# Kernel tuning notes

Hardware: AMD Instinct MI355X
Metric: run time of the kernel (lower is better)

Reference implementation:

```python
import jax, jax.numpy as jnp
import numpy as np

N = 50000          # particles
E = 800000         # edges (avg degree 16)
IN_CH = 64
OUT_CH = 64
KH = 4             # kernel height
KW_HALF = 2        # stored half-width; full width = 4 after antisymmetrization
R = 0.1            # window support radius


def setup_inputs() -> dict:
    key = jax.random.key(0)
    k0, k1, k2, k3, k4 = jax.random.split(key, 5)
    features = jax.random.normal(k0, (N, IN_CH), dtype=jnp.float32)
    receivers = jax.random.randint(k1, (E,), 0, N)
    a = jax.random.randint(k2, (E,), 0, N)  # sender indices
    relative_positions = jax.random.uniform(k3, (E, 2), jnp.float32, -R, R)
    window_support = jnp.float32(R)
    # hk.initializers.RandomUniform(-0.05, 0.05)
    kernel = jax.random.uniform(k4, (KH, KW_HALF, IN_CH, OUT_CH), jnp.float32, -0.05, 0.05)
    bias = jnp.zeros((OUT_CH,), jnp.float32)
    return {"features": features, "receivers": receivers,
            "relative_positions": relative_positions,
            "window_support": window_support, "a": a,
            "kernel": kernel, "bias": bias}


def _continuous_conv(kernel_full, receivers, relative_positions, window_support,
                     features, senders):
    # kernel_full: [kh, kw, in, out]; bilinear interpolation (4 aggregation points)
    kh, kw, in_ch, out_ch = kernel_full.shape
    T = kh * kw
    n = features.shape[0]
    # normalized relative position in [-1, 1]
    u = jnp.clip(relative_positions / window_support, -1.0, 1.0)  # [E,2]
    gx = (u[:, 0] + 1.0) * 0.5 * (kh - 1)
    gy = (u[:, 1] + 1.0) * 0.5 * (kw - 1)
    x0 = jnp.clip(jnp.floor(gx), 0, kh - 2)
    y0 = jnp.clip(jnp.floor(gy), 0, kw - 2)
    fx = gx - x0
    fy = gy - y0
    x0i = x0.astype(jnp.int32)
    y0i = y0.astype(jnp.int32)
    # bilinear corner weights and flat kernel-tap indices  [E,4]
    w = jnp.stack([(1 - fx) * (1 - fy), (1 - fx) * fy,
                   fx * (1 - fy), fx * fy], axis=1)
    taps = jnp.stack([x0i * kw + y0i, x0i * kw + y0i + 1,
                      (x0i + 1) * kw + y0i, (x0i + 1) * kw + y0i + 1], axis=1)
    # smooth window function on normalized radius
    r2 = jnp.sum(u * u, axis=1)
    win = jnp.maximum(1.0 - r2, 0.0) ** 3  # [E]
    # gather sender features, apply window
    g = features[senders] * win[:, None]              # [E,in]
    wf = w[:, :, None] * g[:, None, :]                # [E,4,in]
    # scatter-aggregate into per-(receiver, kernel-tap) buckets
    seg = (receivers[:, None] * T + taps).reshape(-1)  # [E*4]
    A = jax.ops.segment_sum(wf.reshape(-1, in_ch), seg, num_segments=n * T)
    A = A.reshape(n, T, in_ch)
    # contract with kernel taps: out[n,o] = sum_t,i A[n,t,i] K[t,i,o]
    return jnp.einsum('nti,tio->no', A, kernel_full.reshape(T, in_ch, out_ch))


def reference(features, receivers, relative_positions, window_support, a,
              kernel, bias):
    # antisymmetrize kernel: [kh, 2*kw_half, in, out]
    kernel_full = jnp.concatenate([kernel, -jnp.flip(kernel, axis=(0, 1))], axis=1)
    out = _continuous_conv(kernel_full, receivers, relative_positions,
                           window_support, features, a)
    return out + bias
```

## Files before the change

kernel.cpp:

```cpp
#include <hip/hip_runtime.h>
#include <hip/hip_bf16.h>


#define T_TAPS 16
#define BUCKET 64

typedef unsigned short u16;
typedef short s16x8 __attribute__((ext_vector_type(8)));
typedef u16 u16x8 __attribute__((ext_vector_type(8)));
typedef float f32x2 __attribute__((ext_vector_type(2)));
typedef float f32x4 __attribute__((ext_vector_type(4)));

static __device__ __forceinline__ u16 f2bf(float x) {
    union { float f; unsigned u; } v; v.f = x;
    unsigned r = v.u + 0x7FFF + ((v.u >> 16) & 1);
    return (u16)(r >> 16);
}

__global__ __launch_bounds__(256) void ascc_setup(
    u16* __restrict__ KfT, const float* __restrict__ kern,
    int* __restrict__ cnt, int Nn)
{
    int b = blockIdx.x;
    if (b < 256) {
        int idx = b * 256 + threadIdx.x;
        int o = idx >> 10;
        int k = idx & 1023;
        int i = k >> 4, t = k & 15;
        int x = t >> 2, y = t & 3;
        float val;
        if (y < 2) val =  kern[(((x * 2 + y) * 64) + i) * 64 + o];
        else       val = -kern[((((3 - x) * 2 + (3 - y)) * 64) + i) * 64 + o];
        KfT[(size_t)o * 1024 + k] = f2bf(val);
    } else {
        int i = (b - 256) * 256 + threadIdx.x;
        if (i < Nn) cnt[i] = 0;
    }
}

__global__ __launch_bounds__(256) void ascc_fillprep(
    float4* __restrict__ rec,
    int* __restrict__ cnt, const int* __restrict__ receivers,
    const float* __restrict__ relpos, const float* __restrict__ wsup,
    const int* __restrict__ senders, int E)
{
    int e = blockIdx.x * 256 + threadIdx.x;
    if (e >= E) return;
    int r = receivers[e];
    int p = atomicAdd(&cnt[r], 1);
    if (p >= BUCKET) return;

    float ws = wsup[0];
    float2 rp = *(const float2*)(relpos + 2 * e);
    float u0 = fminf(fmaxf(rp.x / ws, -1.f), 1.f);
    float u1 = fminf(fmaxf(rp.y / ws, -1.f), 1.f);
    float gx = (u0 + 1.f) * 1.5f;
    float gy = (u1 + 1.f) * 1.5f;
    float x0f = fminf(fmaxf(floorf(gx), 0.f), 2.f);
    float y0f = fminf(fmaxf(floorf(gy), 0.f), 2.f);
    float fx = gx - x0f, fy = gy - y0f;
    int x0i = (int)x0f, y0i = (int)y0f;
    float r2 = u0 * u0 + u1 * u1;
    float win = fmaxf(1.f - r2, 0.f);
    win = win * win * win;
    float wx[4], wy[4];
    #pragma unroll
    for (int k = 0; k < 4; ++k)
        wx[k] = win * ((k == x0i) ? (1.f - fx) : ((k == x0i + 1) ? fx : 0.f));
    #pragma unroll
    for (int k = 0; k < 4; ++k)
        wy[k] = (k == y0i) ? (1.f - fy) : ((k == y0i + 1) ? fy : 0.f);

    union { int i; float f; } sv; sv.i = senders[e];
    size_t slot = (size_t)r * BUCKET + p;
    rec[2 * slot]     = make_float4(wx[0], wx[1], wx[2], wx[3]);
    rec[2 * slot + 1] = make_float4(wy[0], wy[1], wy[2], sv.f);
}

__global__ __launch_bounds__(256) void ascc_accum(
    u16* __restrict__ Abf,
    const float* __restrict__ features,
    const int* __restrict__ cnt,
    const float4* __restrict__ rec,
    int Nn)
{
    int lane = threadIdx.x & 63;
    int r = blockIdx.x * 4 + (threadIdx.x >> 6);
    if (r >= Nn) return;

    f32x2 acc[8];
    #pragma unroll
    for (int t = 0; t < 8; ++t) acc[t] = (f32x2){0.f, 0.f};

    int n = cnt[r];
    n = (n < BUCKET) ? n : BUCKET;
    const float4* rbase = rec + (size_t)r * (2 * BUCKET);

    #pragma unroll 1
    for (int j = 0; j < n; j += 4) {
        float4 ra[4], rb[4];
        float g[4];
        #pragma unroll
        for (int q = 0; q < 4; ++q) {
            int jj = j + q;
            int jc = (jj < n) ? jj : (n - 1);
            ra[q] = rbase[2 * jc];
            rb[q] = rbase[2 * jc + 1];
        }
        #pragma unroll
        for (int q = 0; q < 4; ++q) {
            union { float f; int i; } sv; sv.f = rb[q].w;
            float gg = features[(size_t)sv.i * 64 + lane];
            g[q] = (j + q < n) ? gg : 0.f;
        }
        #pragma unroll
        for (int q = 0; q < 4; ++q) {
            float wy3 = 1.f - rb[q].x - rb[q].y - rb[q].z;
            f32x2 wyg01 = {rb[q].x * g[q], rb[q].y * g[q]};
            f32x2 wyg23 = {rb[q].z * g[q], wy3 * g[q]};
            float wxa[4] = {ra[q].x, ra[q].y, ra[q].z, ra[q].w};
            #pragma unroll
            for (int tx = 0; tx < 4; ++tx) {
                acc[tx * 2]     += wxa[tx] * wyg01;
                acc[tx * 2 + 1] += wxa[tx] * wyg23;
            }
        }
    }

    u16x8 lo, hi;
    #pragma unroll
    for (int t = 0; t < 8; ++t)  lo[t] = f2bf(acc[(t >> 2) * 2 + ((t & 3) >> 1)][t & 1]);
    #pragma unroll
    for (int t = 0; t < 8; ++t)  hi[t] = f2bf(acc[(2 + (t >> 2)) * 2 + ((t & 3) >> 1)][t & 1]);
    u16* base = Abf + (size_t)r * 1024 + lane * 16;
    *(u16x8*)base = lo;
    *(u16x8*)(base + 8) = hi;
}

__global__ __launch_bounds__(256) void ascc_mgemm(
    float* __restrict__ out,
    const u16* __restrict__ Abf,
    const u16* __restrict__ KfT,
    const float* __restrict__ bias,
    int Nn)
{
    __shared__ u16 Al[64 * 128];
    __shared__ u16 Bl[64 * 128];

    const int tid = threadIdx.x;
    const int lane = tid & 63;
    const int w = tid >> 6;
    const int n0 = blockIdx.x * 64;

    f32x4 acc[4] = {};

    for (int kc = 0; kc < 1024; kc += 128) {
        __syncthreads();
        {
            int row = tid >> 2, seg = tid & 3;
            int n = n0 + row;
            const u16* src = Abf + (size_t)n * 1024 + kc + seg * 32;
            char* dst = (char*)Al + row * 256;
            u16x8 z = {0, 0, 0, 0, 0, 0, 0, 0};
            #pragma unroll
            for (int g2 = 0; g2 < 4; ++g2) {
                u16x8 v = (n < Nn) ? *(const u16x8*)(src + g2 * 8) : z;
                int colb = seg * 64 + g2 * 16;
                *(u16x8*)(dst + (colb ^ ((row & 7) << 4))) = v;
            }
        }
        {
            int row = tid >> 2, seg = tid & 3;
            const u16* src = KfT + (size_t)row * 1024 + kc + seg * 32;
            char* dst = (char*)Bl + row * 256;
            #pragma unroll
            for (int g2 = 0; g2 < 4; ++g2) {
                u16x8 v = *(const u16x8*)(src + g2 * 8);
                int colb = seg * 64 + g2 * 16;
                *(u16x8*)(dst + (colb ^ ((row & 7) << 4))) = v;
            }
        }
        __syncthreads();
        int wr = w << 4;
        #pragma unroll
        for (int ks = 0; ks < 4; ++ks) {
            int arow = wr + (lane & 15);
            int kb = ks * 64 + ((lane >> 4) << 4);
            s16x8 af = *(const s16x8*)((char*)Al + arow * 256 + (kb ^ ((arow & 7) << 4)));
            #pragma unroll
            for (int t = 0; t < 4; ++t) {
                int brow = (t << 4) + (lane & 15);
                s16x8 bf = *(const s16x8*)((char*)Bl + brow * 256 + (kb ^ ((brow & 7) << 4)));
                acc[t] = __builtin_amdgcn_mfma_f32_16x16x32_bf16(af, bf, acc[t], 0, 0, 0);
            }
        }
    }

    int rbase = n0 + (w << 4) + ((lane >> 4) << 2);
    #pragma unroll
    for (int t = 0; t < 4; ++t) {
        int col = (t << 4) + (lane & 15);
        float bv = bias[col];
        #pragma unroll
        for (int reg = 0; reg < 4; ++reg) {
            int n = rbase + reg;
            if (n < Nn) out[(size_t)n * 64 + col] = acc[t][reg] + bv;
        }
    }
}

extern "C" void kernel_launch(void* const* d_in, const int* in_sizes, int n_in,
                              void* d_out, int out_size, void* d_ws, size_t ws_size,
                              hipStream_t stream) {
    const float* features  = (const float*)d_in[0];
    const int*   receivers = (const int*)d_in[1];
    const float* relpos    = (const float*)d_in[2];
    const float* wsup      = (const float*)d_in[3];
    const int*   senders   = (const int*)d_in[4];
    const float* kern      = (const float*)d_in[5];
    const float* bias      = (const float*)d_in[6];
    float* out = (float*)d_out;

    const int Nn = in_sizes[0] / 64;
    const int E  = in_sizes[1];

    char* wp = (char*)d_ws;
    size_t p = 0;
    auto take = [&](size_t bytes) { char* q = wp + p; p = (p + bytes + 255) & ~(size_t)255; return q; };
    int*    cnt = (int*)take((size_t)Nn * 4);
    float4* rec = (float4*)take((size_t)Nn * BUCKET * 32);
    u16*    KfT = (u16*)take((size_t)64 * 1024 * 2);
    u16*    Abf = (u16*)take((size_t)Nn * 1024 * 2);
    (void)ws_size;

    ascc_setup<<<dim3(256 + (Nn + 255) / 256), dim3(256), 0, stream>>>(KfT, kern, cnt, Nn);
    ascc_fillprep<<<dim3((E + 255) / 256), dim3(256), 0, stream>>>(
        rec, cnt, receivers, relpos, wsup, senders, E);
    ascc_accum<<<dim3((Nn + 3) / 4), dim3(256), 0, stream>>>(
        Abf, features, cnt, rec, Nn);
    ascc_mgemm<<<dim3((Nn + 63) / 64), dim3(256), 0, stream>>>(
        out, Abf, KfT, bias, Nn);
}
```

Before: 148.5 us.

## Fuse tap accumulation with MFMA kernel contraction in one kernel

Merges the per-receiver accumulation kernel and the bf16 MFMA GEMM into a single 1024-thread kernel. Each wave builds one receiver row of the accumulated tap matrix directly into swizzled LDS, then four waves run the 16-row GEMM reading kernel fragments straight from global memory. This removes the round trip of the ~100 MB bf16 intermediate through HBM and one kernel launch. In exchange, 12 of 16 waves sit idle during the GEMM, the B operand is re-read from global/L2 per block without LDS staging, and the large blocks with 32 KB of LDS may lower occupancy.

```diff
diff --git a/kernel.cpp b/kernel.cpp
--- a/kernel.cpp
+++ b/kernel.cpp
@@ -77,134 +77,108 @@
     rec[2 * slot + 1] = make_float4(wy[0], wy[1], wy[2], sv.f);
 }
 
-__global__ __launch_bounds__(256) void ascc_accum(
-    u16* __restrict__ Abf,
+__global__ __launch_bounds__(1024) void ascc_fused(
+    float* __restrict__ out,
     const float* __restrict__ features,
     const int* __restrict__ cnt,
     const float4* __restrict__ rec,
-    int Nn)
-{
-    int lane = threadIdx.x & 63;
-    int r = blockIdx.x * 4 + (threadIdx.x >> 6);
-    if (r >= Nn) return;
-
-    f32x2 acc[8];
-    #pragma unroll
-    for (int t = 0; t < 8; ++t) acc[t] = (f32x2){0.f, 0.f};
-
-    int n = cnt[r];
-    n = (n < BUCKET) ? n : BUCKET;
-    const float4* rbase = rec + (size_t)r * (2 * BUCKET);
-
-    #pragma unroll 1
-    for (int j = 0; j < n; j += 4) {
-        float4 ra[4], rb[4];
-        float g[4];
-        #pragma unroll
-        for (int q = 0; q < 4; ++q) {
-            int jj = j + q;
-            int jc = (jj < n) ? jj : (n - 1);
-            ra[q] = rbase[2 * jc];
-            rb[q] = rbase[2 * jc + 1];
-        }
-        #pragma unroll
-        for (int q = 0; q < 4; ++q) {
-            union { float f; int i; } sv; sv.f = rb[q].w;
-            float gg = features[(size_t)sv.i * 64 + lane];
-            g[q] = (j + q < n) ? gg : 0.f;
-        }
-        #pragma unroll
-        for (int q = 0; q < 4; ++q) {
-            float wy3 = 1.f - rb[q].x - rb[q].y - rb[q].z;
-            f32x2 wyg01 = {rb[q].x * g[q], rb[q].y * g[q]};
-            f32x2 wyg23 = {rb[q].z * g[q], wy3 * g[q]};
-            float wxa[4] = {ra[q].x, ra[q].y, ra[q].z, ra[q].w};
-            #pragma unroll
-            for (int tx = 0; tx < 4; ++tx) {
-                acc[tx * 2]     += wxa[tx] * wyg01;
-                acc[tx * 2 + 1] += wxa[tx] * wyg23;
-            }
-        }
-    }
-
-    u16x8 lo, hi;
-    #pragma unroll
-    for (int t = 0; t < 8; ++t)  lo[t] = f2bf(acc[(t >> 2) * 2 + ((t & 3) >> 1)][t & 1]);
-    #pragma unroll
-    for (int t = 0; t < 8; ++t)  hi[t] = f2bf(acc[(2 + (t >> 2)) * 2 + ((t & 3) >> 1)][t & 1]);
-    u16* base = Abf + (size_t)r * 1024 + lane * 16;
-    *(u16x8*)base = lo;
-    *(u16x8*)(base + 8) = hi;
-}
-
-__global__ __launch_bounds__(256) void ascc_mgemm(
-    float* __restrict__ out,
-    const u16* __restrict__ Abf,
     const u16* __restrict__ KfT,
     const float* __restrict__ bias,
     int Nn)
 {
-    __shared__ u16 Al[64 * 128];
-    __shared__ u16 Bl[64 * 128];
-
-    const int tid = threadIdx.x;
+    __shared__ u16 Al[16 * 1024];
+
+    const int tid  = threadIdx.x;
     const int lane = tid & 63;
-    const int w = tid >> 6;
-    const int n0 = blockIdx.x * 64;
-
-    f32x4 acc[4] = {};
-
-    for (int kc = 0; kc < 1024; kc += 128) {
-        __syncthreads();
-        {
-            int row = tid >> 2, seg = tid & 3;
-            int n = n0 + row;
-            const u16* src = Abf + (size_t)n * 1024 + kc + seg * 32;
-            char* dst = (char*)Al + row * 256;
-            u16x8 z = {0, 0, 0, 0, 0, 0, 0, 0};
+    const int w    = tid >> 6;
+    const int n0   = blockIdx.x * 16;
+    const int row  = w;
+    const int r    = n0 + row;
+    const int sw   = (row & 7) << 4;
+    char* lbase = (char*)Al + row * 2048;
+
+    if (r >= Nn) {
+        u16x8 z = {0, 0, 0, 0, 0, 0, 0, 0};
+        *(u16x8*)(lbase + ((lane * 32) ^ sw)) = z;
+        *(u16x8*)(lbase + ((lane * 32 + 16) ^ sw)) = z;
+    } else {
+        f32x2 acc[8];
+        #pragma unroll
+        for (int t = 0; t < 8; ++t) acc[t] = (f32x2){0.f, 0.f};
+
+        int n = cnt[r];
+        n = (n < BUCKET) ? n : BUCKET;
+        const float4* rbase = rec + (size_t)r * (2 * BUCKET);
+
+        #pragma unroll 1
+        for (int j = 0; j < n; j += 4) {
+            float4 ra[4], rb[4];
+            float g[4];
             #pragma unroll
-            for (int g2 = 0; g2 < 4; ++g2) {
-                u16x8 v = (n < Nn) ? *(const u16x8*)(src + g2 * 8) : z;
-                int colb = seg * 64 + g2 * 16;
-                *(u16x8*)(dst + (colb ^ ((row & 7) << 4))) = v;
+            for (int q = 0; q < 4; ++q) {
+                int jj = j + q;
+                int jc = (jj < n) ? jj : (n - 1);
+                ra[q] = rbase[2 * jc];
+                rb[q] = rbase[2 * jc + 1];
+            }
+            #pragma unroll
+            for (int q = 0; q < 4; ++q) {
+                union { float f; int i; } sv; sv.f = rb[q].w;
+                float gg = features[(size_t)sv.i * 64 + lane];
+                g[q] = (j + q < n) ? gg : 0.f;
+            }
+            #pragma unroll
+            for (int q = 0; q < 4; ++q) {
+                float wy3 = 1.f - rb[q].x - rb[q].y - rb[q].z;
+                f32x2 wyg01 = {rb[q].x * g[q], rb[q].y * g[q]};
+                f32x2 wyg23 = {rb[q].z * g[q], wy3 * g[q]};
+                float wxa[4] = {ra[q].x, ra[q].y, ra[q].z, ra[q].w};
+                #pragma unroll
+                for (int tx = 0; tx < 4; ++tx) {
+                    acc[tx * 2]     += wxa[tx] * wyg01;
+                    acc[tx * 2 + 1] += wxa[tx] * wyg23;
+                }
             }
         }
-        {
-            int row = tid >> 2, seg = tid & 3;
-            const u16* src = KfT + (size_t)row * 1024 + kc + seg * 32;
-            char* dst = (char*)Bl + row * 256;
-            #pragma unroll
-            for (int g2 = 0; g2 < 4; ++g2) {
-                u16x8 v = *(const u16x8*)(src + g2 * 8);
-                int colb = seg * 64 + g2 * 16;
-                *(u16x8*)(dst + (colb ^ ((row & 7) << 4))) = v;
-            }
+
+        u16x8 lo, hi;
+        #pragma unroll
+        for (int t = 0; t < 8; ++t)  lo[t] = f2bf(acc[(t >> 2) * 2 + ((t & 3) >> 1)][t & 1]);
+        #pragma unroll
+        for (int t = 0; t < 8; ++t)  hi[t] = f2bf(acc[(2 + (t >> 2)) * 2 + ((t & 3) >> 1)][t & 1]);
+        *(u16x8*)(lbase + ((lane * 32) ^ sw)) = lo;
+        *(u16x8*)(lbase + ((lane * 32 + 16) ^ sw)) = hi;
+    }
+
+    __syncthreads();
+
+    if (w < 4) {
+        const int arow  = lane & 15;
+        const int asw   = (arow & 7) << 4;
+        const char* ab  = (const char*)Al + arow * 2048;
+        const int kfrag = (lane >> 4) << 3;
+        const u16* bptr = KfT + (size_t)((w << 4) + (lane & 15)) * 1024 + kfrag;
+
+        f32x4 c0 = {}, c1 = {};
+        #pragma unroll
+        for (int kc = 0; kc < 1024; kc += 64) {
+            int kb0 = (kc + kfrag) << 1;
+            int kb1 = (kc + 32 + kfrag) << 1;
+            s16x8 af0 = *(const s16x8*)(ab + (kb0 ^ asw));
+            s16x8 af1 = *(const s16x8*)(ab + (kb1 ^ asw));
+            s16x8 bf0 = *(const s16x8*)(bptr + kc);
+            s16x8 bf1 = *(const s16x8*)(bptr + kc + 32);
+            c0 = __builtin_amdgcn_mfma_f32_16x16x32_bf16(af0, bf0, c0, 0, 0, 0);
+            c1 = __builtin_amdgcn_mfma_f32_16x16x32_bf16(af1, bf1, c1, 0, 0, 0);
         }
-        __syncthreads();
-        int wr = w << 4;
-        #pragma unroll
-        for (int ks = 0; ks < 4; ++ks) {
-            int arow = wr + (lane & 15);
-            int kb = ks * 64 + ((lane >> 4) << 4);
-            s16x8 af = *(const s16x8*)((char*)Al + arow * 256 + (kb ^ ((arow & 7) << 4)));
-            #pragma unroll
-            for (int t = 0; t < 4; ++t) {
-                int brow = (t << 4) + (lane & 15);
-                s16x8 bf = *(const s16x8*)((char*)Bl + brow * 256 + (kb ^ ((brow & 7) << 4)));
-                acc[t] = __builtin_amdgcn_mfma_f32_16x16x32_bf16(af, bf, acc[t], 0, 0, 0);
-            }
-        }
-    }
-
-    int rbase = n0 + (w << 4) + ((lane >> 4) << 2);
-    #pragma unroll
-    for (int t = 0; t < 4; ++t) {
-        int col = (t << 4) + (lane & 15);
-        float bv = bias[col];
+
+        const int col = (w << 4) + (lane & 15);
+        const float bv = bias[col];
+        const int drow = (lane >> 4) << 2;
         #pragma unroll
         for (int reg = 0; reg < 4; ++reg) {
-            int n = rbase + reg;
-            if (n < Nn) out[(size_t)n * 64 + col] = acc[t][reg] + bv;
+            int nn = n0 + drow + reg;
+            if (nn < Nn) out[(size_t)nn * 64 + col] = c0[reg] + c1[reg] + bv;
         }
     }
 }
@@ -230,14 +204,11 @@
     int*    cnt = (int*)take((size_t)Nn * 4);
     float4* rec = (float4*)take((size_t)Nn * BUCKET * 32);
     u16*    KfT = (u16*)take((size_t)64 * 1024 * 2);
-    u16*    Abf = (u16*)take((size_t)Nn * 1024 * 2);
     (void)ws_size;
 
     ascc_setup<<<dim3(256 + (Nn + 255) / 256), dim3(256), 0, stream>>>(KfT, kern, cnt, Nn);
     ascc_fillprep<<<dim3((E + 255) / 256), dim3(256), 0, stream>>>(
         rec, cnt, receivers, relpos, wsup, senders, E);
-    ascc_accum<<<dim3((Nn + 3) / 4), dim3(256), 0, stream>>>(
-        Abf, features, cnt, rec, Nn);
-    ascc_mgemm<<<dim3((Nn + 63) / 64), dim3(256), 0, stream>>>(
-        out, Abf, KfT, bias, Nn);
-}
+    ascc_fused<<<dim3((Nn + 15) / 16), dim3(1024), 0, stream>>>(
+        out, features, cnt, rec, KfT, bias, Nn);
+}
```

Result: slower. 168.8 us (+13.7%).
